# Optimization experiments

Measured on AMD Instinct MI355X. Metric: run time of the kernel, lower is better.

## Reference

```python
import jax, jax.numpy as jnp
import numpy as np

N_NODES = 20000
N_EDGES = 640000
HIDDEN = 256
D_OP = 140
D_EMB = 64
D_CFG = 52
OP_SIZE = 120
EPS = 1e-5


def layer_norm(x, gamma, beta):
    mu = jnp.mean(x, axis=-1, keepdims=True)
    var = jnp.mean(jnp.square(x - mu), axis=-1, keepdims=True)
    return (x - mu) * jax.lax.rsqrt(var + EPS) * gamma + beta


def setup_inputs() -> dict:
    key = jax.random.key(0)
    ks = list(jax.random.split(key, 32))
    nk = iter(ks).__next__
    s = 1.0 / np.sqrt(HIDDEN)
    inp = {
        "op_feats": jax.random.normal(nk(), (N_NODES, D_OP), jnp.float32),
        "config_feats": jax.random.normal(nk(), (N_NODES, D_CFG), jnp.float32),
        "embed_table": jax.random.normal(nk(), (OP_SIZE, D_EMB), jnp.float32) * 0.1,
        "feat_mean": jax.random.normal(nk(), (HIDDEN,), jnp.float32) * 0.1,
        "feat_std": jax.random.uniform(nk(), (HIDDEN,), jnp.float32, 0.5, 1.5),
        # 4 stacked SAGEConv layers (mean aggregator)
        "Wself": jax.random.normal(nk(), (4, HIDDEN, HIDDEN), jnp.float32) * s,
        "Wneigh": jax.random.normal(nk(), (4, HIDDEN, HIDDEN), jnp.float32) * s,
        "bconv": jnp.zeros((4, HIDDEN), jnp.float32),
        "conv_gamma": jnp.ones((4, HIDDEN), jnp.float32),
        "conv_beta": jnp.zeros((4, HIDDEN), jnp.float32),
        # end_mlp head
        "W1": jax.random.normal(nk(), (HIDDEN, HIDDEN), jnp.float32) * s,
        "g1": jnp.ones((HIDDEN,), jnp.float32),
        "b1": jnp.zeros((HIDDEN,), jnp.float32),
        "W2": jax.random.normal(nk(), (HIDDEN, HIDDEN // 2), jnp.float32) * s,
        "g2": jnp.ones((HIDDEN // 2,), jnp.float32),
        "b2": jnp.zeros((HIDDEN // 2,), jnp.float32),
        # graph structure
        "op_ids": jax.random.randint(nk(), (N_NODES,), 0, OP_SIZE, jnp.int32),
        "src": jax.random.randint(nk(), (N_EDGES,), 0, N_NODES, jnp.int32),
        "dst": jax.random.randint(nk(), (N_EDGES,), 0, N_NODES, jnp.int32),
    }
    return inp


def reference(op_feats, config_feats, embed_table, feat_mean, feat_std,
              Wself, Wneigh, bconv, conv_gamma, conv_beta,
              W1, g1, b1, W2, g2, b2, op_ids, src, dst):
    # op embedding + feature concat, then (x - mean) / std normalization
    op_e = embed_table[op_ids]                                   # [N, 64]
    x = jnp.concatenate([op_feats, op_e, config_feats], axis=-1)  # [N, 256]
    x = (x - feat_mean) / feat_std

    # in-degree for mean aggregation (graph is fixed across layers)
    deg = jax.ops.segment_sum(jnp.ones((N_EDGES,), x.dtype), dst,
                              num_segments=N_NODES)
    inv_deg = (1.0 / jnp.maximum(deg, 1.0))[:, None]             # [N, 1]

    for i in range(4):
        msg = x[src]                                             # [E, 256] gather
        agg = jax.ops.segment_sum(msg, dst, num_segments=N_NODES) * inv_deg
        h = x @ Wself[i] + agg @ Wneigh[i] + bconv[i]
        x = jax.nn.relu(layer_norm(h, conv_gamma[i], conv_beta[i]))

    # end_mlp: Dense(256, no bias) -> norm -> relu -> Dense(128, no bias) -> norm -> relu
    h = jax.nn.relu(layer_norm(x @ W1, g1, b1))
    h = jax.nn.relu(layer_norm(h @ W2, g2, b2))
    return h                                                      # [N, 128]
```

## Files before the change

kernel.cpp:

```cpp
#include <hip/hip_runtime.h>
#include <hip/hip_bf16.h>
#include <string.h>

#define N_NODES 20000
#define N_EDGES 640000
#define HID 256
#define D_OP 140
#define D_EMB 64
#define D_CFG 52
#define LDX 512

typedef short bf16x8 __attribute__((ext_vector_type(8)));
typedef short bf16x4 __attribute__((ext_vector_type(4)));
typedef float f32x4 __attribute__((ext_vector_type(4)));

typedef __hip_bfloat16 bf16;

__device__ inline float b2f(short s) {
    unsigned int u = ((unsigned int)(unsigned short)s) << 16;
    float f; __builtin_memcpy(&f, &u, 4); return f;
}
__device__ inline short f2b(float f) {
    __hip_bfloat16 h = __float2bfloat16(f);
    short s; __builtin_memcpy(&s, &h, 2); return s;
}

__global__ __launch_bounds__(256) void embed_kernel(
    const float* __restrict__ op_feats, const float* __restrict__ cfg,
    const float* __restrict__ emb, const float* __restrict__ mean,
    const float* __restrict__ stdv, const int* __restrict__ op_ids,
    bf16* __restrict__ X2)
{
    int n = blockIdx.x;
    int j = threadIdx.x;
    float v;
    if (j < D_OP)              v = op_feats[(size_t)n * D_OP + j];
    else if (j < D_OP + D_EMB) v = emb[(size_t)op_ids[n] * D_EMB + (j - D_OP)];
    else                       v = cfg[(size_t)n * D_CFG + (j - D_OP - D_EMB)];
    X2[(size_t)n * LDX + j] = __float2bfloat16((v - mean[j]) / stdv[j]);
}

__global__ __launch_bounds__(256) void build_wt(
    const float* __restrict__ Wself, const float* __restrict__ Wneigh,
    const float* __restrict__ W1, const float* __restrict__ W2,
    bf16* __restrict__ WTc, bf16* __restrict__ W1T, bf16* __restrict__ W2T)
{
    int idx = blockIdx.x * 256 + threadIdx.x;
    const int NC = 4 * 256 * 512;
    if (idx < NC) {
        int l = idx >> 17;
        int rem = idx & 131071;
        int n = rem >> 9;
        int k = rem & 511;
        float v = (k < 256) ? Wself[l * 65536 + k * 256 + n]
                            : Wneigh[l * 65536 + (k - 256) * 256 + n];
        WTc[idx] = __float2bfloat16(v);
    } else if (idx < NC + 65536) {
        int i = idx - NC;
        int n = i >> 8, k = i & 255;
        W1T[i] = __float2bfloat16(W1[k * 256 + n]);
    } else if (idx < NC + 65536 + 32768) {
        int i = idx - NC - 65536;
        int n = i >> 8, k = i & 255;
        W2T[i] = __float2bfloat16(W2[k * 128 + n]);
    }
}

__global__ __launch_bounds__(256) void deg_kernel(const int* __restrict__ dst, int* __restrict__ deg)
{
    int e = blockIdx.x * 256 + threadIdx.x;
    if (e < N_EDGES) atomicAdd(&deg[dst[e]], 1);
}

__global__ __launch_bounds__(1024) void scan_kernel(const int* __restrict__ deg, int* __restrict__ row_off)
{
    __shared__ int sdata[1024];
    int t = threadIdx.x;
    int base = t * 20;
    int local[20];
    int s = 0;
#pragma unroll
    for (int i = 0; i < 20; i++) {
        int idx = base + i;
        local[i] = (idx < N_NODES) ? deg[idx] : 0;
        s += local[i];
    }
    sdata[t] = s;
    __syncthreads();
    for (int off = 1; off < 1024; off <<= 1) {
        int v = (t >= off) ? sdata[t - off] : 0;
        __syncthreads();
        sdata[t] += v;
        __syncthreads();
    }
    int run = sdata[t] - s;
#pragma unroll
    for (int i = 0; i < 20; i++) {
        int idx = base + i;
        if (idx < N_NODES) { row_off[idx] = run; run += local[i]; }
    }
    if (t == 1023) row_off[N_NODES] = sdata[1023];
}

__global__ __launch_bounds__(256) void prep_kernel(const int* __restrict__ deg,
    const int* __restrict__ row_off, int* __restrict__ cursor, float* __restrict__ inv_deg)
{
    int n = blockIdx.x * 256 + threadIdx.x;
    if (n < N_NODES) {
        cursor[n] = row_off[n];
        inv_deg[n] = 1.0f / fmaxf((float)deg[n], 1.0f);
    }
}

__global__ __launch_bounds__(256) void fill_kernel(const int* __restrict__ src,
    const int* __restrict__ dst, int* __restrict__ cursor, int* __restrict__ ssrc)
{
    int e = blockIdx.x * 256 + threadIdx.x;
    if (e < N_EDGES) {
        int d = dst[e];
        int pos = atomicAdd(&cursor[d], 1);
        ssrc[pos] = src[e];
    }
}

__global__ __launch_bounds__(256) void agg_kernel(const bf16* __restrict__ X2,
    const int* __restrict__ row_off, const int* __restrict__ ssrc,
    const float* __restrict__ inv_deg, bf16* __restrict__ X2w)
{
    const int wid = threadIdx.x >> 6;
    const int lane = threadIdx.x & 63;
    const int n = blockIdx.x * 4 + wid;
    if (n >= N_NODES) return;
    const int e0 = row_off[n], e1 = row_off[n + 1];
    const size_t fo = (size_t)lane * 4;
    float a0 = 0.f, a1 = 0.f, a2 = 0.f, a3 = 0.f;
    int e = e0;
    for (; e + 1 < e1; e += 2) {
        int s0 = ssrc[e], s1 = ssrc[e + 1];
        bf16x4 v0 = *reinterpret_cast<const bf16x4*>(X2 + (size_t)s0 * LDX + fo);
        bf16x4 v1 = *reinterpret_cast<const bf16x4*>(X2 + (size_t)s1 * LDX + fo);
        a0 += b2f(v0.x) + b2f(v1.x);
        a1 += b2f(v0.y) + b2f(v1.y);
        a2 += b2f(v0.z) + b2f(v1.z);
        a3 += b2f(v0.w) + b2f(v1.w);
    }
    if (e < e1) {
        int s0 = ssrc[e];
        bf16x4 v0 = *reinterpret_cast<const bf16x4*>(X2 + (size_t)s0 * LDX + fo);
        a0 += b2f(v0.x); a1 += b2f(v0.y); a2 += b2f(v0.z); a3 += b2f(v0.w);
    }
    const float id = inv_deg[n];
    bf16x4 o;
    o.x = f2b(a0 * id); o.y = f2b(a1 * id); o.z = f2b(a2 * id); o.w = f2b(a3 * id);
    *reinterpret_cast<bf16x4*>(X2w + (size_t)n * LDX + fo) = o;
}

template <int NT, int KDIM, typename OutT>
__global__ __launch_bounds__(256) void gemm_ln_relu(
    const bf16* __restrict__ A, int lda,
    const bf16* __restrict__ WT,
    const float* __restrict__ bias,
    const float* __restrict__ gamma, const float* __restrict__ beta,
    OutT* __restrict__ out, int ldo, int M)
{
    constexpr int NCOLS = NT * 16;
    constexpr int BK = 64;
    constexpr int NCHUNK = KDIM / BK;
    __shared__ __align__(16) short Bs[2][NCOLS][72];

    const int wid = threadIdx.x >> 6;
    const int lane = threadIdx.x & 63;
    const int r0 = blockIdx.x * 64 + wid * 16;
    const int lr = lane & 15;
    const int kg = lane >> 4;

    f32x4 acc[NT];
#pragma unroll
    for (int i = 0; i < NT; i++) acc[i] = (f32x4){0.f, 0.f, 0.f, 0.f};

    const int arow_idx = (r0 + lr < M) ? (r0 + lr) : (M - 1);
    const bf16* arow = A + (size_t)arow_idx * lda + kg * 8;

    auto stage = [&](int buf, int kbase) {
#pragma unroll
        for (int c = threadIdx.x; c < NCOLS * 8; c += 256) {
            int n = c >> 3, slot = c & 7;
            bf16x8 v = *reinterpret_cast<const bf16x8*>(WT + (size_t)n * KDIM + kbase + slot * 8);
            *reinterpret_cast<bf16x8*>(&Bs[buf][n][slot * 8]) = v;
        }
    };

    bf16x8 aCur0 = *reinterpret_cast<const bf16x8*>(arow);
    bf16x8 aCur1 = *reinterpret_cast<const bf16x8*>(arow + 32);
    stage(0, 0);
    __syncthreads();

    for (int c = 0; c < NCHUNK; ++c) {
        bf16x8 aN0, aN1;
        if (c + 1 < NCHUNK) {
            stage((c + 1) & 1, (c + 1) * BK);
            aN0 = *reinterpret_cast<const bf16x8*>(arow + (c + 1) * BK);
            aN1 = *reinterpret_cast<const bf16x8*>(arow + (c + 1) * BK + 32);
        }
        const int buf = c & 1;
#pragma unroll
        for (int nt = 0; nt < NT; ++nt) {
            const short* bp = &Bs[buf][nt * 16 + lr][kg * 8];
            bf16x8 b0 = *reinterpret_cast<const bf16x8*>(bp);
            bf16x8 b1 = *reinterpret_cast<const bf16x8*>(bp + 32);
            acc[nt] = __builtin_amdgcn_mfma_f32_16x16x32_bf16(aCur0, b0, acc[nt], 0, 0, 0);
            acc[nt] = __builtin_amdgcn_mfma_f32_16x16x32_bf16(aCur1, b1, acc[nt], 0, 0, 0);
        }
        if (c + 1 < NCHUNK) { aCur0 = aN0; aCur1 = aN1; }
        __syncthreads();
    }

    const float Nf = (float)NCOLS;
    float sum[4] = {0, 0, 0, 0}, sq[4] = {0, 0, 0, 0};
#pragma unroll
    for (int nt = 0; nt < NT; nt++) {
        int col = nt * 16 + lr;
        float bv = bias ? bias[col] : 0.0f;
#pragma unroll
        for (int r = 0; r < 4; r++) {
            float v = acc[nt][r] + bv;
            acc[nt][r] = v;
            sum[r] += v;
            sq[r] += v * v;
        }
    }
#pragma unroll
    for (int m = 1; m < 16; m <<= 1) {
#pragma unroll
        for (int r = 0; r < 4; r++) {
            sum[r] += __shfl_xor(sum[r], m, 64);
            sq[r]  += __shfl_xor(sq[r], m, 64);
        }
    }
    float mean_[4], rstd[4];
#pragma unroll
    for (int r = 0; r < 4; r++) {
        float mu = sum[r] / Nf;
        float var = sq[r] / Nf - mu * mu;
        mean_[r] = mu;
        rstd[r] = rsqrtf(var + 1e-5f);
    }
#pragma unroll
    for (int nt = 0; nt < NT; nt++) {
        int col = nt * 16 + lr;
        float g = gamma[col];
        float be = beta[col];
#pragma unroll
        for (int r = 0; r < 4; r++) {
            int row = r0 + kg * 4 + r;
            if (row < M) {
                float v = (acc[nt][r] - mean_[r]) * rstd[r] * g + be;
                v = fmaxf(v, 0.0f);
                if constexpr (__is_same(OutT, float)) {
                    out[(size_t)row * ldo + col] = v;
                } else {
                    out[(size_t)row * ldo + col] = __float2bfloat16(v);
                }
            }
        }
    }
}

extern "C" void kernel_launch(void* const* d_in, const int* in_sizes, int n_in,
                              void* d_out, int out_size, void* d_ws, size_t ws_size,
                              hipStream_t stream)
{
    const float* op_feats     = (const float*)d_in[0];
    const float* config_feats = (const float*)d_in[1];
    const float* embed_table  = (const float*)d_in[2];
    const float* feat_mean    = (const float*)d_in[3];
    const float* feat_std     = (const float*)d_in[4];
    const float* Wself        = (const float*)d_in[5];
    const float* Wneigh       = (const float*)d_in[6];
    const float* bconv        = (const float*)d_in[7];
    const float* conv_gamma   = (const float*)d_in[8];
    const float* conv_beta    = (const float*)d_in[9];
    const float* W1           = (const float*)d_in[10];
    const float* g1           = (const float*)d_in[11];
    const float* b1           = (const float*)d_in[12];
    const float* W2           = (const float*)d_in[13];
    const float* g2           = (const float*)d_in[14];
    const float* b2           = (const float*)d_in[15];
    const int* op_ids = (const int*)d_in[16];
    const int* src    = (const int*)d_in[17];
    const int* dst    = (const int*)d_in[18];

    char* w = (char*)d_ws;
    auto alloc = [&](size_t bytes) -> void* {
        void* p = (void*)w;
        w += (bytes + 255) & ~(size_t)255;
        return p;
    };
    bf16* X2  = (bf16*)alloc((size_t)N_NODES * LDX * 2);
    bf16* WTc = (bf16*)alloc((size_t)4 * 256 * 512 * 2);
    bf16* W1T = (bf16*)alloc((size_t)256 * 256 * 2);
    bf16* W2T = (bf16*)alloc((size_t)128 * 256 * 2);
    int* deg     = (int*)alloc((size_t)N_NODES * 4);
    int* row_off = (int*)alloc((size_t)(N_NODES + 1) * 4);
    int* cursor  = (int*)alloc((size_t)N_NODES * 4);
    float* inv_deg = (float*)alloc((size_t)N_NODES * 4);
    int* ssrc    = (int*)alloc((size_t)N_EDGES * 4);

    float* out = (float*)d_out;

    hipMemsetAsync(deg, 0, (size_t)N_NODES * 4, stream);

    build_wt<<<2432, 256, 0, stream>>>(Wself, Wneigh, W1, W2, WTc, W1T, W2T);
    embed_kernel<<<N_NODES, 256, 0, stream>>>(op_feats, config_feats, embed_table,
                                              feat_mean, feat_std, op_ids, X2);
    deg_kernel<<<(N_EDGES + 255) / 256, 256, 0, stream>>>(dst, deg);
    scan_kernel<<<1, 1024, 0, stream>>>(deg, row_off);
    prep_kernel<<<(N_NODES + 255) / 256, 256, 0, stream>>>(deg, row_off, cursor, inv_deg);
    fill_kernel<<<(N_EDGES + 255) / 256, 256, 0, stream>>>(src, dst, cursor, ssrc);

    const int GEMM_GRID = (N_NODES + 63) / 64;
    const int AGG_GRID  = (N_NODES + 3) / 4;

    for (int l = 0; l < 4; ++l) {
        agg_kernel<<<AGG_GRID, 256, 0, stream>>>(X2, row_off, ssrc, inv_deg, X2 + 256);
        gemm_ln_relu<16, 512, bf16><<<GEMM_GRID, 256, 0, stream>>>(
            X2, LDX, WTc + (size_t)l * 256 * 512,
            bconv + (size_t)l * 256, conv_gamma + (size_t)l * 256, conv_beta + (size_t)l * 256,
            X2, LDX, N_NODES);
    }
    gemm_ln_relu<16, 256, bf16><<<GEMM_GRID, 256, 0, stream>>>(
        X2, LDX, W1T, (const float*)nullptr, g1, b1, X2 + 256, LDX, N_NODES);
    gemm_ln_relu<8, 256, float><<<GEMM_GRID, 256, 0, stream>>>(
        X2 + 256, LDX, W2T, (const float*)nullptr, g2, b2, out, 128, N_NODES);
    (void)ws_size; (void)n_in; (void)in_sizes; (void)out_size;
}
```

Baseline: 590.0 us.

## Split edge loop across half-waves and register-stage weight tiles in GEMM

The aggregation kernel now splits each node's edges between two half-waves. Each lane loads 8 bf16 values per neighbor, and the two halves' partial sums are combined with a cross-lane shuffle. This widens the loads and doubles the number of outstanding gathers per wave. The GEMM kernel now loads the next weight chunk into registers before the MFMA loop and writes it to LDS only after the MFMAs, so the global load latency overlaps with compute instead of stalling before it. The trade-offs are higher register pressure in the GEMM and half the lanes sitting idle during the aggregation store.

```diff
diff --git a/kernel.cpp b/kernel.cpp
--- a/kernel.cpp
+++ b/kernel.cpp
@@ -129,30 +129,39 @@
 {
     const int wid = threadIdx.x >> 6;
     const int lane = threadIdx.x & 63;
+    const int half = lane >> 5;
+    const int hl = lane & 31;
     const int n = blockIdx.x * 4 + wid;
     if (n >= N_NODES) return;
     const int e0 = row_off[n], e1 = row_off[n + 1];
-    const size_t fo = (size_t)lane * 4;
-    float a0 = 0.f, a1 = 0.f, a2 = 0.f, a3 = 0.f;
-    int e = e0;
-    for (; e + 1 < e1; e += 2) {
-        int s0 = ssrc[e], s1 = ssrc[e + 1];
-        bf16x4 v0 = *reinterpret_cast<const bf16x4*>(X2 + (size_t)s0 * LDX + fo);
-        bf16x4 v1 = *reinterpret_cast<const bf16x4*>(X2 + (size_t)s1 * LDX + fo);
-        a0 += b2f(v0.x) + b2f(v1.x);
-        a1 += b2f(v0.y) + b2f(v1.y);
-        a2 += b2f(v0.z) + b2f(v1.z);
-        a3 += b2f(v0.w) + b2f(v1.w);
+    const size_t fo = (size_t)hl * 8;
+    float a[8] = {0.f, 0.f, 0.f, 0.f, 0.f, 0.f, 0.f, 0.f};
+
+    int e = e0 + half;
+    while (e + 2 < e1) {
+        int s0 = ssrc[e], s1 = ssrc[e + 2];
+        bf16x8 v0 = *reinterpret_cast<const bf16x8*>(X2 + (size_t)s0 * LDX + fo);
+        bf16x8 v1 = *reinterpret_cast<const bf16x8*>(X2 + (size_t)s1 * LDX + fo);
+#pragma unroll
+        for (int j = 0; j < 8; j++) a[j] += b2f(v0[j]) + b2f(v1[j]);
+        e += 4;
     }
     if (e < e1) {
         int s0 = ssrc[e];
-        bf16x4 v0 = *reinterpret_cast<const bf16x4*>(X2 + (size_t)s0 * LDX + fo);
-        a0 += b2f(v0.x); a1 += b2f(v0.y); a2 += b2f(v0.z); a3 += b2f(v0.w);
-    }
-    const float id = inv_deg[n];
-    bf16x4 o;
-    o.x = f2b(a0 * id); o.y = f2b(a1 * id); o.z = f2b(a2 * id); o.w = f2b(a3 * id);
-    *reinterpret_cast<bf16x4*>(X2w + (size_t)n * LDX + fo) = o;
+        bf16x8 v0 = *reinterpret_cast<const bf16x8*>(X2 + (size_t)s0 * LDX + fo);
+#pragma unroll
+        for (int j = 0; j < 8; j++) a[j] += b2f(v0[j]);
+    }
+#pragma unroll
+    for (int j = 0; j < 8; j++) a[j] += __shfl_xor(a[j], 32, 64);
+
+    if (half == 0) {
+        const float id = inv_deg[n];
+        bf16x8 o;
+#pragma unroll
+        for (int j = 0; j < 8; j++) o[j] = f2b(a[j] * id);
+        *reinterpret_cast<bf16x8*>(X2w + (size_t)n * LDX + fo) = o;
+    }
 }
 
 template <int NT, int KDIM, typename OutT>
@@ -166,6 +175,7 @@
     constexpr int NCOLS = NT * 16;
     constexpr int BK = 64;
     constexpr int NCHUNK = KDIM / BK;
+    constexpr int SREG = NT / 2;
     __shared__ __align__(16) short Bs[2][NCOLS][72];
 
     const int wid = threadIdx.x >> 6;
@@ -181,28 +191,38 @@
     const int arow_idx = (r0 + lr < M) ? (r0 + lr) : (M - 1);
     const bf16* arow = A + (size_t)arow_idx * lda + kg * 8;
 
-    auto stage = [&](int buf, int kbase) {
-#pragma unroll
-        for (int c = threadIdx.x; c < NCOLS * 8; c += 256) {
-            int n = c >> 3, slot = c & 7;
-            bf16x8 v = *reinterpret_cast<const bf16x8*>(WT + (size_t)n * KDIM + kbase + slot * 8);
-            *reinterpret_cast<bf16x8*>(&Bs[buf][n][slot * 8]) = v;
+    bf16x8 sreg[SREG];
+    auto issue = [&](int kbase) {
+#pragma unroll
+        for (int i = 0; i < SREG; ++i) {
+            int c = threadIdx.x + i * 256;
+            int nrow = c >> 3, slot = c & 7;
+            sreg[i] = *reinterpret_cast<const bf16x8*>(WT + (size_t)nrow * KDIM + kbase + slot * 8);
         }
     };
-
+    auto commit = [&](int buf) {
+#pragma unroll
+        for (int i = 0; i < SREG; ++i) {
+            int c = threadIdx.x + i * 256;
+            int nrow = c >> 3, slot = c & 7;
+            *reinterpret_cast<bf16x8*>(&Bs[buf][nrow][slot * 8]) = sreg[i];
+        }
+    };
+
+    issue(0);
     bf16x8 aCur0 = *reinterpret_cast<const bf16x8*>(arow);
     bf16x8 aCur1 = *reinterpret_cast<const bf16x8*>(arow + 32);
-    stage(0, 0);
+    commit(0);
     __syncthreads();
 
     for (int c = 0; c < NCHUNK; ++c) {
+        const int buf = c & 1;
         bf16x8 aN0, aN1;
         if (c + 1 < NCHUNK) {
-            stage((c + 1) & 1, (c + 1) * BK);
+            issue((c + 1) * BK);
             aN0 = *reinterpret_cast<const bf16x8*>(arow + (c + 1) * BK);
             aN1 = *reinterpret_cast<const bf16x8*>(arow + (c + 1) * BK + 32);
         }
-        const int buf = c & 1;
 #pragma unroll
         for (int nt = 0; nt < NT; ++nt) {
             const short* bp = &Bs[buf][nt * 16 + lr][kg * 8];
@@ -211,7 +231,10 @@
             acc[nt] = __builtin_amdgcn_mfma_f32_16x16x32_bf16(aCur0, b0, acc[nt], 0, 0, 0);
             acc[nt] = __builtin_amdgcn_mfma_f32_16x16x32_bf16(aCur1, b1, acc[nt], 0, 0, 0);
         }
-        if (c + 1 < NCHUNK) { aCur0 = aN0; aCur1 = aN1; }
+        if (c + 1 < NCHUNK) {
+            commit(buf ^ 1);
+            aCur0 = aN0; aCur1 = aN1;
+        }
         __syncthreads();
     }
 
```

After: 472.2 us. -20.0%, faster.
